# Performance work log

Hardware: AMD Instinct MI355X
Metric: run time of the kernel (lower is better)

Reference implementation:

```python
import jax, jax.numpy as jnp
import numpy as np

WS = 7  # window_size


def _conv1x1(x, W, b):
    # 1x1 conv == channel-mixing matmul. W: [out_c, in_c], b: [out_c]
    return jnp.einsum('oc,bchw->bohw', W, x) + b[None, :, None, None]


def _window_flatten(t, ws):
    # [b, ch, H, W] -> [b, ch*nh*nw, ws*ws], matching torch unfold+contiguous+view
    b, ch, H, W = t.shape
    nh, nw = H // ws, W // ws
    t = t.reshape(b, ch, nh, ws, nw, ws).transpose(0, 1, 2, 4, 3, 5)  # [b,ch,nh,nw,ws,ws]
    return t.reshape(b, ch * nh * nw, ws * ws)


def setup_inputs() -> dict:
    key = jax.random.key(0)
    ks = jax.random.split(key, 7)
    b, c, h, w = 8, 256, 160, 160
    c8 = c // 8
    x = jax.random.normal(ks[0], (b, c, h, w), dtype=jnp.float32)
    Wq = jax.random.normal(ks[1], (c8, c), dtype=jnp.float32) * (1.0 / np.sqrt(c))
    bq = jnp.zeros((c8,), dtype=jnp.float32)
    Wk = jax.random.normal(ks[2], (c8, c), dtype=jnp.float32) * (1.0 / np.sqrt(c))
    bk = jnp.zeros((c8,), dtype=jnp.float32)
    Wv = jax.random.normal(ks[3], (c, c), dtype=jnp.float32) * (1.0 / np.sqrt(c))
    bv = jnp.zeros((c,), dtype=jnp.float32)
    return {"x": x, "Wq": Wq, "bq": bq, "Wk": Wk, "bk": bk, "Wv": Wv, "bv": bv}


def reference(x, Wq, bq, Wk, bk, Wv, bv):
    b, c, h, w = x.shape
    ws = WS
    pad_h = (ws - h % ws) % ws
    pad_w = (ws - w % ws) % ws
    xp = jnp.pad(x, ((0, 0), (0, 0), (0, pad_h), (0, pad_w)), mode='reflect')
    H, W = xp.shape[2], xp.shape[3]

    q = _window_flatten(_conv1x1(xp, Wq, bq), ws)  # [b, c8*nwin, 49]
    k = _window_flatten(_conv1x1(xp, Wk, bk), ws)  # [b, c8*nwin, 49]
    v = _window_flatten(_conv1x1(xp, Wv, bv), ws)  # [b, c*nwin, 49]

    # attn = softmax(q^T @ k) over last dim; reduction axis is channels*windows
    attn = jax.nn.softmax(jnp.einsum('bnp,bnq->bpq', q, k), axis=-1)  # [b,49,49]
    # out = v @ attn^T  -> out[b,m,i] = sum_j v[b,m,j] * attn[b,i,j]
    out = jnp.einsum('bmj,bij->bmi', v, attn)  # [b, c*nwin, 49]

    # faithful to torch .view(b, c, H, W) on contiguous [b,c,nh,nw,ws,ws] memory
    out = out.reshape(b, c, H, W)
    return out[:, :, :h, :w]
```

## Files before the change

kernel.cpp:

```cpp
#include <hip/hip_runtime.h>

#define C_ 256
#define HIN 160
#define NH 23
#define NWIN 529
#define G5 5
#define NGRP 106
#define OPLANE 25600

typedef short bf16x8 __attribute__((ext_vector_type(8)));
typedef float f32x4 __attribute__((ext_vector_type(4)));
typedef unsigned short u16x4 __attribute__((ext_vector_type(4)));

__device__ __forceinline__ unsigned short f2bf(float f) {
    union { float f; unsigned u; } v; v.f = f;
    unsigned r = v.u + 0x7FFFu + ((v.u >> 16) & 1u);
    return (unsigned short)(r >> 16);
}

__global__ void kprep(const float* __restrict__ Wq, const float* __restrict__ Wk,
                      const float* __restrict__ Wv, unsigned short* __restrict__ WvB,
                      float* __restrict__ W2t) {
    int t = blockIdx.x * 256 + threadIdx.x;
    if (t < 65536) WvB[t] = f2bf(Wv[t]);
    if (t < 16384) {
        int c = t >> 6, ch = t & 63;
        W2t[c * 64 + ch] = (ch < 32) ? Wq[ch * 256 + c] : Wk[(ch - 32) * 256 + c];
    }
}

#define QST 260
#define XST 264
__launch_bounds__(256, 2)
__global__ void k12(const float* __restrict__ x, const float* __restrict__ W2t,
                    const float* __restrict__ bq, const float* __restrict__ bk,
                    float* __restrict__ Spart) {
    __shared__ float QKs[64 * QST];
    __shared__ float Xs[8 * XST];
    __shared__ float Ws[8 * 64];

    int t = threadIdx.x;
    int g = blockIdx.x;
    int b = g & 7;
    int grp = g >> 3;
    int win0 = grp * G5;

    int wloc = t / 49, p = t % 49;
    int win = win0 + wloc;
    bool pxvalid = (t < 245) && (win < NWIN);
    const float* xp = x;
    if (pxvalid) {
        int wy = win / NH, wx = win % NH;
        int gy = wy * 7 + p / 7, gx = wx * 7 + p % 7;
        int sy = (gy < HIN) ? gy : 158;
        int sx = (gx < HIN) ? gx : 158;
        xp = x + (long)b * C_ * OPLANE + sy * HIN + sx;
    }

    int tx = t & 31, ty = t >> 5;

    float acc[8][8];
#pragma unroll
    for (int i = 0; i < 8; ++i)
#pragma unroll
        for (int j = 0; j < 8; ++j) acc[i][j] = 0.f;

    float prefX[8], prefW[2];
#pragma unroll
    for (int e = 0; e < 8; ++e) prefX[e] = pxvalid ? xp[(long)e * OPLANE] : 0.f;
#pragma unroll
    for (int i = 0; i < 2; ++i) {
        int idx = i * 256 + t, e = idx >> 6, ch = idx & 63;
        prefW[i] = W2t[e * 64 + ch];
    }

    for (int c0 = 0; c0 < 256; c0 += 8) {
#pragma unroll
        for (int e = 0; e < 8; ++e) Xs[e * XST + t] = prefX[e];
#pragma unroll
        for (int i = 0; i < 2; ++i) {
            int idx = i * 256 + t, e = idx >> 6, ch = idx & 63;
            Ws[e * 64 + ch] = prefW[i];
        }
        __syncthreads();
        if (c0 + 8 < 256) {
            int c1 = c0 + 8;
#pragma unroll
            for (int e = 0; e < 8; ++e) prefX[e] = pxvalid ? xp[(long)(c1 + e) * OPLANE] : 0.f;
#pragma unroll
            for (int i = 0; i < 2; ++i) {
                int idx = i * 256 + t, e = idx >> 6, ch = idx & 63;
                prefW[i] = W2t[(c1 + e) * 64 + ch];
            }
        }
#pragma unroll
        for (int kk = 0; kk < 8; ++kk) {
            float wv[8], xv[8];
#pragma unroll
            for (int i = 0; i < 8; ++i) wv[i] = Ws[kk * 64 + ty * 8 + i];
#pragma unroll
            for (int i = 0; i < 8; ++i) xv[i] = Xs[kk * XST + tx * 8 + i];
#pragma unroll
            for (int ci = 0; ci < 8; ++ci)
#pragma unroll
                for (int pi = 0; pi < 8; ++pi)
                    acc[ci][pi] = fmaf(wv[ci], xv[pi], acc[ci][pi]);
        }
        __syncthreads();
    }

    bool cvalid[8];
#pragma unroll
    for (int pi = 0; pi < 8; ++pi) {
        int px = tx * 8 + pi;
        int w = px / 49;
        cvalid[pi] = (px < 245) && (win0 + w < NWIN);
    }
    const float* bb = (ty < 4) ? (bq + ty * 8) : (bk + (ty - 4) * 8);
    float bias[8];
#pragma unroll
    for (int ci = 0; ci < 8; ++ci) bias[ci] = bb[ci];
#pragma unroll
    for (int ci = 0; ci < 8; ++ci) {
        int ch = ty * 8 + ci;
#pragma unroll
        for (int pi = 0; pi < 8; ++pi) {
            int px = tx * 8 + pi;
            QKs[ch * QST + px] = cvalid[pi] ? (acc[ci][pi] + bias[ci]) : 0.f;
        }
    }
    __syncthreads();

    if (t < 169) {
        int p0 = (t / 13) * 4, q0 = (t % 13) * 4;
        float s[4][4];
#pragma unroll
        for (int r = 0; r < 4; ++r)
#pragma unroll
            for (int cc = 0; cc < 4; ++cc) s[r][cc] = 0.f;
        for (int w = 0; w < G5; ++w) {
            for (int ch = 0; ch < 32; ++ch) {
                const float* qr = &QKs[ch * QST + w * 49 + p0];
                const float* kr = &QKs[(32 + ch) * QST + w * 49 + q0];
                float qv[4] = {qr[0], qr[1], qr[2], qr[3]};
                float kv[4] = {kr[0], kr[1], kr[2], kr[3]};
#pragma unroll
                for (int r = 0; r < 4; ++r)
#pragma unroll
                    for (int cc = 0; cc < 4; ++cc)
                        s[r][cc] = fmaf(qv[r], kv[cc], s[r][cc]);
            }
        }
        float* sp = Spart + (long)(b * NGRP + grp) * 2401;
#pragma unroll
        for (int r = 0; r < 4; ++r) {
            int pp = p0 + r;
            if (pp < 49) {
#pragma unroll
                for (int cc = 0; cc < 4; ++cc) {
                    int qq = q0 + cc;
                    if (qq < 49) sp[pp * 49 + qq] = s[r][cc];
                }
            }
        }
    }
}

__global__ void kred(const float* __restrict__ Spart, float* __restrict__ S) {
    int tg = blockIdx.x * 256 + threadIdx.x;
    if (tg >= 8 * 2401) return;
    int b = tg / 2401, idx = tg % 2401;
    float s = 0.f;
    for (int gr = 0; gr < NGRP; ++gr) s += Spart[(long)(b * NGRP + gr) * 2401 + idx];
    S[b * 2401 + idx] = s;
}

__global__ void ksoft(const float* __restrict__ S, unsigned short* __restrict__ attnP) {
    int b = blockIdx.x, t = threadIdx.x;
    unsigned short* row = attnP + (b * 64 + t) * 64;
    if (t < 49) {
        const float* sr = S + b * 2401 + t * 49;
        float m = -1e30f;
        for (int j = 0; j < 49; ++j) m = fmaxf(m, sr[j]);
        float den = 0.f;
        for (int j = 0; j < 49; ++j) den += expf(sr[j] - m);
        float inv = 1.f / den;
        for (int j = 0; j < 49; ++j) row[j] = f2bf(expf(sr[j] - m) * inv);
        for (int j = 49; j < 64; ++j) row[j] = 0;
    } else {
        for (int j = 0; j < 64; ++j) row[j] = 0;
    }
}

__launch_bounds__(256, 3)
__global__ void k3(const float* __restrict__ x, const unsigned short* __restrict__ WvB,
                   const unsigned short* __restrict__ attnP, const float* __restrict__ bv,
                   float* __restrict__ out) {
    __shared__ __align__(16) unsigned short Xc[256 * 40];
    __shared__ __align__(16) unsigned short Yt[64 * 264];

    int t = threadIdx.x;
    int bw = blockIdx.x;
    int b = bw & 7;
    int win = bw >> 3;
    int wy = win / NH, wx = win % NH;
    int lane = t & 63;
    int r16 = lane & 15, quad = lane >> 4, q8 = quad * 8;
    int w64 = (t >> 6) * 64;

    f32x4 zero = {0.f, 0.f, 0.f, 0.f};
    f32x4 acc1[4][4];
#pragma unroll
    for (int i = 0; i < 4; ++i)
#pragma unroll
        for (int j = 0; j < 4; ++j) acc1[i][j] = zero;

    const float* xb = x + (long)b * C_ * OPLANE;

    for (int half = 0; half < 2; ++half) {
        int jbase = half * 32;
        for (int idx = t; idx < 256 * 32; idx += 256) {
            int c = idx >> 5, j0 = idx & 31, j = jbase + j0;
            float v = 0.f;
            if (j < 49) {
                int gy = wy * 7 + j / 7, gx = wx * 7 + j % 7;
                int sy = (gy < HIN) ? gy : 158;
                int sx = (gx < HIN) ? gx : 158;
                v = xb[c * OPLANE + sy * HIN + sx];
            }
            Xc[c * 40 + j0] = f2bf(v);
        }
        __syncthreads();

        int k0 = jbase;
        bf16x8 a[4], bfr[4];
#pragma unroll
        for (int mt = 0; mt < 4; ++mt)
            a[mt] = *(const bf16x8*)&Xc[(w64 + mt * 16 + r16) * 40 + q8];
#pragma unroll
        for (int nt = 0; nt < 4; ++nt)
            bfr[nt] = *(const bf16x8*)&attnP[(b * 64 + nt * 16 + r16) * 64 + k0 + q8];
#pragma unroll
        for (int mt = 0; mt < 4; ++mt)
#pragma unroll
            for (int nt = 0; nt < 4; ++nt)
                acc1[mt][nt] = __builtin_amdgcn_mfma_f32_16x16x32_bf16(a[mt], bfr[nt], acc1[mt][nt], 0, 0, 0);
        __syncthreads();
    }

#pragma unroll
    for (int mt = 0; mt < 4; ++mt) {
        int cb = w64 + mt * 16 + quad * 4;
#pragma unroll
        for (int nt = 0; nt < 4; ++nt) {
            int ic = nt * 16 + r16;
            u16x4 pk;
            pk[0] = f2bf(acc1[mt][nt][0]);
            pk[1] = f2bf(acc1[mt][nt][1]);
            pk[2] = f2bf(acc1[mt][nt][2]);
            pk[3] = f2bf(acc1[mt][nt][3]);
            *(u16x4*)&Yt[ic * 264 + cb] = pk;
        }
    }
    __syncthreads();

    f32x4 acc2[4][4];
#pragma unroll
    for (int i = 0; i < 4; ++i)
#pragma unroll
        for (int j = 0; j < 4; ++j) acc2[i][j] = zero;

#pragma unroll
    for (int ks = 0; ks < 8; ++ks) {
        int k0 = ks * 32;
        bf16x8 a[4], bb2[4];
#pragma unroll
        for (int mt = 0; mt < 4; ++mt)
            a[mt] = *(const bf16x8*)&WvB[(w64 + mt * 16 + r16) * 256 + k0 + q8];
#pragma unroll
        for (int nt = 0; nt < 4; ++nt)
            bb2[nt] = *(const bf16x8*)&Yt[(nt * 16 + r16) * 264 + k0 + q8];
#pragma unroll
        for (int mt = 0; mt < 4; ++mt)
#pragma unroll
            for (int nt = 0; nt < 4; ++nt)
                acc2[mt][nt] = __builtin_amdgcn_mfma_f32_16x16x32_bf16(a[mt], bb2[nt], acc2[mt][nt], 0, 0, 0);
    }

    float* ob = out + (long)b * C_ * OPLANE;
#pragma unroll
    for (int nt = 0; nt < 4; ++nt) {
        int i = nt * 16 + r16;
        if (i >= 49) continue;
        int f = win * 49 + i;
        int y = f / 161, xcol = f % 161;
        if (y >= 160 || xcol >= 160) continue;
        int dst = y * 160 + xcol;
#pragma unroll
        for (int mt = 0; mt < 4; ++mt) {
            int cb = w64 + mt * 16 + quad * 4;
#pragma unroll
            for (int r = 0; r < 4; ++r) {
                int ch = cb + r;
                ob[ch * OPLANE + dst] = acc2[mt][nt][r] + bv[ch];
            }
        }
    }
}

extern "C" void kernel_launch(void* const* d_in, const int* in_sizes, int n_in,
                              void* d_out, int out_size, void* d_ws, size_t ws_size,
                              hipStream_t stream) {
    const float* x  = (const float*)d_in[0];
    const float* Wq = (const float*)d_in[1];
    const float* bq = (const float*)d_in[2];
    const float* Wk = (const float*)d_in[3];
    const float* bk = (const float*)d_in[4];
    const float* Wv = (const float*)d_in[5];
    const float* bv = (const float*)d_in[6];
    float* out = (float*)d_out;

    char* ws = (char*)d_ws;
    unsigned short* WvB   = (unsigned short*)(ws);
    float* W2t            = (float*)(ws + 131072);
    float* Spart          = (float*)(ws + 196608);
    float* S              = (float*)(ws + 196608 + 8144192);
    unsigned short* attnP = (unsigned short*)(ws + 196608 + 8144192 + 76832);

    kprep<<<dim3(256), dim3(256), 0, stream>>>(Wq, Wk, Wv, WvB, W2t);
    k12<<<dim3(8 * NGRP), dim3(256), 0, stream>>>(x, W2t, bq, bk, Spart);
    kred<<<dim3(76), dim3(256), 0, stream>>>(Spart, S);
    ksoft<<<dim3(8), dim3(64), 0, stream>>>(S, attnP);
    k3<<<dim3(8 * NWIN), dim3(256), 0, stream>>>(x, WvB, attnP, bv, out);
}
```

Before: 741.3 us.

## Alias k3 LDS buffers, single-pass X gather, and stage output through LDS for coalesced stores

k3 now loads the whole 256x64 window tile into LDS in a single pass, with each thread keeping a fixed pixel and walking channels, instead of two half passes. The Xc, Yt and a new fp32 output staging buffer share one LDS allocation. Together with reusing one accumulator array, this cuts LDS and register footprint so launch bounds can go from 3 to 4 blocks. The output is transposed through LDS in two 128-channel halves so consecutive threads write consecutive pixels of a channel plane, replacing scattered per-channel stores, at the cost of extra barriers.

```diff
diff --git a/kernel.cpp b/kernel.cpp
--- a/kernel.cpp
+++ b/kernel.cpp
@@ -192,12 +192,17 @@
     }
 }
 
-__launch_bounds__(256, 3)
+#define XCS 72
+#define YTS 264
+#define OTS 65
+__launch_bounds__(256, 4)
 __global__ void k3(const float* __restrict__ x, const unsigned short* __restrict__ WvB,
                    const unsigned short* __restrict__ attnP, const float* __restrict__ bv,
                    float* __restrict__ out) {
-    __shared__ __align__(16) unsigned short Xc[256 * 40];
-    __shared__ __align__(16) unsigned short Yt[64 * 264];
+    __shared__ __align__(16) unsigned short U[256 * XCS];
+    unsigned short* Xc = U;
+    unsigned short* Yt = U;
+    float* Ot = (float*)U;
 
     int t = threadIdx.x;
     int bw = blockIdx.x;
@@ -208,35 +213,37 @@
     int r16 = lane & 15, quad = lane >> 4, q8 = quad * 8;
     int w64 = (t >> 6) * 64;
 
+    const float* xb = x + (long)b * C_ * OPLANE;
+
+    {
+        int j = t & 63;
+        bool jvalid = (j < 49);
+        int gy = wy * 7 + j / 7, gx = wx * 7 + j % 7;
+        int sy = (gy < HIN) ? gy : 158;
+        int sx = (gx < HIN) ? gx : 158;
+        const float* xs = xb + sy * HIN + sx;
+#pragma unroll 4
+        for (int c = (t >> 6); c < 256; c += 4) {
+            float v = jvalid ? xs[(long)c * OPLANE] : 0.f;
+            Xc[c * XCS + j] = f2bf(v);
+        }
+    }
+    __syncthreads();
+
     f32x4 zero = {0.f, 0.f, 0.f, 0.f};
-    f32x4 acc1[4][4];
+    f32x4 acc[4][4];
 #pragma unroll
     for (int i = 0; i < 4; ++i)
 #pragma unroll
-        for (int j = 0; j < 4; ++j) acc1[i][j] = zero;
-
-    const float* xb = x + (long)b * C_ * OPLANE;
-
+        for (int j = 0; j < 4; ++j) acc[i][j] = zero;
+
+#pragma unroll
     for (int half = 0; half < 2; ++half) {
-        int jbase = half * 32;
-        for (int idx = t; idx < 256 * 32; idx += 256) {
-            int c = idx >> 5, j0 = idx & 31, j = jbase + j0;
-            float v = 0.f;
-            if (j < 49) {
-                int gy = wy * 7 + j / 7, gx = wx * 7 + j % 7;
-                int sy = (gy < HIN) ? gy : 158;
-                int sx = (gx < HIN) ? gx : 158;
-                v = xb[c * OPLANE + sy * HIN + sx];
-            }
-            Xc[c * 40 + j0] = f2bf(v);
-        }
-        __syncthreads();
-
-        int k0 = jbase;
+        int k0 = half * 32;
         bf16x8 a[4], bfr[4];
 #pragma unroll
         for (int mt = 0; mt < 4; ++mt)
-            a[mt] = *(const bf16x8*)&Xc[(w64 + mt * 16 + r16) * 40 + q8];
+            a[mt] = *(const bf16x8*)&Xc[(w64 + mt * 16 + r16) * XCS + k0 + q8];
 #pragma unroll
         for (int nt = 0; nt < 4; ++nt)
             bfr[nt] = *(const bf16x8*)&attnP[(b * 64 + nt * 16 + r16) * 64 + k0 + q8];
@@ -244,9 +251,9 @@
         for (int mt = 0; mt < 4; ++mt)
 #pragma unroll
             for (int nt = 0; nt < 4; ++nt)
-                acc1[mt][nt] = __builtin_amdgcn_mfma_f32_16x16x32_bf16(a[mt], bfr[nt], acc1[mt][nt], 0, 0, 0);
-        __syncthreads();
-    }
+                acc[mt][nt] = __builtin_amdgcn_mfma_f32_16x16x32_bf16(a[mt], bfr[nt], acc[mt][nt], 0, 0, 0);
+    }
+    __syncthreads();
 
 #pragma unroll
     for (int mt = 0; mt < 4; ++mt) {
@@ -255,20 +262,19 @@
         for (int nt = 0; nt < 4; ++nt) {
             int ic = nt * 16 + r16;
             u16x4 pk;
-            pk[0] = f2bf(acc1[mt][nt][0]);
-            pk[1] = f2bf(acc1[mt][nt][1]);
-            pk[2] = f2bf(acc1[mt][nt][2]);
-            pk[3] = f2bf(acc1[mt][nt][3]);
-            *(u16x4*)&Yt[ic * 264 + cb] = pk;
-        }
-    }
-    __syncthreads();
-
-    f32x4 acc2[4][4];
+            pk[0] = f2bf(acc[mt][nt][0]);
+            pk[1] = f2bf(acc[mt][nt][1]);
+            pk[2] = f2bf(acc[mt][nt][2]);
+            pk[3] = f2bf(acc[mt][nt][3]);
+            *(u16x4*)&Yt[ic * YTS + cb] = pk;
+        }
+    }
+    __syncthreads();
+
 #pragma unroll
     for (int i = 0; i < 4; ++i)
 #pragma unroll
-        for (int j = 0; j < 4; ++j) acc2[i][j] = zero;
+        for (int j = 0; j < 4; ++j) acc[i][j] = zero;
 
 #pragma unroll
     for (int ks = 0; ks < 8; ++ks) {
@@ -279,32 +285,47 @@
             a[mt] = *(const bf16x8*)&WvB[(w64 + mt * 16 + r16) * 256 + k0 + q8];
 #pragma unroll
         for (int nt = 0; nt < 4; ++nt)
-            bb2[nt] = *(const bf16x8*)&Yt[(nt * 16 + r16) * 264 + k0 + q8];
+            bb2[nt] = *(const bf16x8*)&Yt[(nt * 16 + r16) * YTS + k0 + q8];
 #pragma unroll
         for (int mt = 0; mt < 4; ++mt)
 #pragma unroll
             for (int nt = 0; nt < 4; ++nt)
-                acc2[mt][nt] = __builtin_amdgcn_mfma_f32_16x16x32_bf16(a[mt], bb2[nt], acc2[mt][nt], 0, 0, 0);
-    }
+                acc[mt][nt] = __builtin_amdgcn_mfma_f32_16x16x32_bf16(a[mt], bb2[nt], acc[mt][nt], 0, 0, 0);
+    }
+    __syncthreads();
 
     float* ob = out + (long)b * C_ * OPLANE;
-#pragma unroll
-    for (int nt = 0; nt < 4; ++nt) {
-        int i = nt * 16 + r16;
-        if (i >= 49) continue;
-        int f = win * 49 + i;
-        int y = f / 161, xcol = f % 161;
-        if (y >= 160 || xcol >= 160) continue;
-        int dst = y * 160 + xcol;
-#pragma unroll
-        for (int mt = 0; mt < 4; ++mt) {
-            int cb = w64 + mt * 16 + quad * 4;
-#pragma unroll
-            for (int r = 0; r < 4; ++r) {
-                int ch = cb + r;
-                ob[ch * OPLANE + dst] = acc2[mt][nt][r] + bv[ch];
-            }
-        }
+    int f0 = win * 49;
+    int y0 = f0 / 161, x0 = f0 - y0 * 161;
+#pragma unroll
+    for (int h = 0; h < 2; ++h) {
+        if ((w64 >> 7) == h) {
+#pragma unroll
+            for (int mt = 0; mt < 4; ++mt) {
+                int clb = (w64 & 127) + mt * 16 + quad * 4;
+#pragma unroll
+                for (int nt = 0; nt < 4; ++nt) {
+                    int i = nt * 16 + r16;
+                    if (i < 49) {
+#pragma unroll
+                        for (int r = 0; r < 4; ++r)
+                            Ot[(clb + r) * OTS + i] = acc[mt][nt][r];
+                    }
+                }
+            }
+        }
+        __syncthreads();
+        for (int idx = t; idx < 128 * 49; idx += 256) {
+            int cl = idx / 49;
+            int jj = idx - cl * 49;
+            int xx = x0 + jj, yy = y0;
+            if (xx >= 161) { ++yy; xx -= 161; }
+            if (xx < 160 && yy < 160) {
+                int ch = h * 128 + cl;
+                ob[ch * OPLANE + yy * 160 + xx] = Ot[cl * OTS + jj] + bv[ch];
+            }
+        }
+        __syncthreads();
     }
 }
 
```

Result: no change. 731.4 us (-1.3%).
